# Kernel tuning notes

Measured on AMD Instinct MI355X. Metric: run time of the kernel, lower is better.

Reference implementation:

```python
import jax, jax.numpy as jnp
import numpy as np
from jax import lax

DN = ('NCHW', 'HWIO', 'NCHW')

def conv(x, w, b, stride, pad):
    y = lax.conv_general_dilated(x, w, (stride, stride), ((pad, pad), (pad, pad)),
                                 dimension_numbers=DN)
    return y + b[None, :, None, None]

def deconv(x, w, b):
    # PyTorch ConvTranspose2d(k=4, s=2, p=1) == conv with lhs_dilation=2, padding=k-1-p=2
    y = lax.conv_general_dilated(x, w, (1, 1), ((2, 2), (2, 2)), lhs_dilation=(2, 2),
                                 dimension_numbers=DN)
    return y + b[None, :, None, None]

def setup_inputs() -> dict:
    key = jax.random.key(0)
    ks = jax.random.split(key, 16)
    B, K, D = 4096, 512, 64
    def w(k, shape, fan_in):
        s = 1.0 / np.sqrt(fan_in)
        return jax.random.uniform(k, shape, jnp.float32, -s, s)
    return {
        'x': jax.random.uniform(ks[0], (B, 1, 28, 28), jnp.float32),
        # encoder
        'w1': w(ks[1], (4, 4, 1, 32), 4 * 4 * 1),  'b1': w(ks[2], (32,), 4 * 4 * 1),
        'w2': w(ks[3], (4, 4, 32, 64), 4 * 4 * 32), 'b2': w(ks[4], (64,), 4 * 4 * 32),
        'w3': w(ks[5], (1, 1, 64, D), 64),          'b3': w(ks[6], (D,), 64),
        # codebook, init uniform(-1/K, 1/K) as in the torch module
        'codebook': jax.random.uniform(ks[7], (K, D), jnp.float32, -1.0 / K, 1.0 / K),
        # decoder
        'dw0': w(ks[8], (1, 1, D, 64), D),          'db0': w(ks[9], (64,), D),
        'dw1': w(ks[10], (4, 4, 64, 32), 4 * 4 * 64), 'db1': w(ks[11], (32,), 4 * 4 * 64),
        'dw2': w(ks[12], (4, 4, 32, 1), 4 * 4 * 32),  'db2': w(ks[13], (1,), 4 * 4 * 32),
    }

def vector_quantize(z_perm, codebook, commitment_cost=0.25):
    # z_perm: [B, H, W, D]
    D = codebook.shape[1]
    flat_z = z_perm.reshape(-1, D)                                      # [N, D]
    dists = (jnp.sum(flat_z * flat_z, axis=1, keepdims=True)
             + jnp.sum(codebook * codebook, axis=1)
             - 2.0 * flat_z @ codebook.T)                               # [N, K]
    indices = jnp.argmin(dists, axis=1)                                 # [N]
    quantized = codebook[indices].reshape(z_perm.shape)                 # [B, H, W, D]
    e_latent = jnp.mean((quantized - lax.stop_gradient(z_perm)) ** 2)
    q_latent = jnp.mean((z_perm - lax.stop_gradient(quantized)) ** 2)
    vq_loss = e_latent + commitment_cost * q_latent
    quantized_st = z_perm + lax.stop_gradient(quantized - z_perm)
    return quantized_st, vq_loss, indices.reshape(z_perm.shape[:-1])

def reference(x, w1, b1, w2, b2, w3, b3, codebook, dw0, db0, dw1, db1, dw2, db2):
    # encoder: 28 -> 14 -> 7
    h = jax.nn.relu(conv(x, w1, b1, 2, 1))
    h = jax.nn.relu(conv(h, w2, b2, 2, 1))
    z = conv(h, w3, b3, 1, 0)                        # [B, D, 7, 7]
    z_perm = jnp.transpose(z, (0, 2, 3, 1))          # [B, 7, 7, D]
    zq_perm, vq_loss, indices = vector_quantize(z_perm, codebook)
    z_q = jnp.transpose(zq_perm, (0, 3, 1, 2))       # [B, D, 7, 7]
    # decoder: 7 -> 14 -> 28
    d = conv(z_q, dw0, db0, 1, 0)
    d = jax.nn.relu(deconv(d, dw1, db1))
    recon = jax.nn.sigmoid(deconv(d, dw2, db2))
    recon = recon[:, :, :28, :28]
    return recon, z, z_q, vq_loss, indices
```

## Files before the change

### kernel.cpp

```cpp
#include <hip/hip_runtime.h>


#define NB 4096

__device__ __forceinline__ float4 f4fma(float s, float4 w, float4 a) {
  a.x = fmaf(s, w.x, a.x); a.y = fmaf(s, w.y, a.y);
  a.z = fmaf(s, w.z, a.z); a.w = fmaf(s, w.w, a.w);
  return a;
}
__device__ __forceinline__ float4 f4relu(float4 a) {
  a.x = fmaxf(a.x, 0.f); a.y = fmaxf(a.y, 0.f);
  a.z = fmaxf(a.z, 0.f); a.w = fmaxf(a.w, 0.f);
  return a;
}
__device__ __forceinline__ float4 f4addrn(float4 a, float4 b) {
  a.x = __fadd_rn(a.x, b.x); a.y = __fadd_rn(a.y, b.y);
  a.z = __fadd_rn(a.z, b.z); a.w = __fadd_rn(a.w, b.w);
  return a;
}

__device__ __forceinline__ float np_sumsq64(const float* v) {
  float r[8];
#pragma unroll
  for (int j = 0; j < 8; ++j) r[j] = __fmul_rn(v[j], v[j]);
#pragma unroll
  for (int i = 8; i < 64; i += 8)
#pragma unroll
    for (int j = 0; j < 8; ++j) r[j] = __fadd_rn(r[j], __fmul_rn(v[i + j], v[i + j]));
  return __fadd_rn(__fadd_rn(__fadd_rn(r[0], r[1]), __fadd_rn(r[2], r[3])),
                   __fadd_rn(__fadd_rn(r[4], r[5]), __fadd_rn(r[6], r[7])));
}

__global__ __launch_bounds__(256) void k0_init(const float* __restrict__ cb,
                                               float* __restrict__ cn,
                                               float* __restrict__ loss) {
  int t = threadIdx.x;
  if (t == 0) *loss = 0.f;
  for (int k = t; k < 512; k += 256) cn[k] = np_sumsq64(&cb[k * 64]);
}

__global__ __launch_bounds__(256) void k1_conv1(const float* __restrict__ x,
                                                const float* __restrict__ w1,
                                                const float* __restrict__ b1,
                                                float* __restrict__ h1) {
  __shared__ float xs[784];
  __shared__ float wl[512];
  __shared__ float bs[32];
  int n = blockIdx.x, t = threadIdx.x;
  for (int j = t; j < 784; j += 256) xs[j] = x[n * 784 + j];
  for (int j = t; j < 512; j += 256) wl[j] = w1[j];
  if (t < 32) bs[t] = b1[t];
  __syncthreads();
  int c = t & 31, pg = t >> 5;
  for (int s = pg; s < 196; s += 8) {
    int oh = s / 14, ow = s % 14;
    float acc = 0.f;
#pragma unroll
    for (int kh = 0; kh < 4; ++kh) {
      int ih = 2 * oh - 1 + kh;
      if (ih < 0 || ih >= 28) continue;
#pragma unroll
      for (int kw = 0; kw < 4; ++kw) {
        int iw = 2 * ow - 1 + kw;
        if (iw < 0 || iw >= 28) continue;
        acc = fmaf(xs[ih * 28 + iw], wl[(kh * 4 + kw) * 32 + c], acc);
      }
    }
    acc = __fadd_rn(acc, bs[c]);
    h1[(n * 196 + s) * 32 + c] = fmaxf(acc, 0.f);
  }
}

__global__ __launch_bounds__(256) void k2_conv2(const float* __restrict__ h1,
                                                const float* __restrict__ w2,
                                                const float* __restrict__ b2,
                                                float* __restrict__ h2) {
  __shared__ float4 xs4[2 * 2049];
  int nb = blockIdx.x, t = threadIdx.x;
  size_t n0 = (size_t)nb * 2;
  for (int j = t; j < 4098; j += 256) xs4[j] = make_float4(0.f, 0.f, 0.f, 0.f);
  __syncthreads();
  for (int j = t; j < 1568; j += 256) {
    int p = j >> 3, c4 = j & 7;
    int ihp = p / 14 + 1, iwp = p % 14 + 1;
    int chunk = (c4 * 16 + ihp) * 16 + (iwp & 1) * 8 + (iwp >> 1);
    xs4[chunk] = *(const float4*)(h1 + n0 * 6272 + p * 32 + c4 * 4);
    xs4[2049 + chunk] = *(const float4*)(h1 + (n0 + 1) * 6272 + p * 32 + c4 * 4);
  }
  __syncthreads();
  int l = t & 63;
  int co0 = __builtin_amdgcn_readfirstlane((t >> 6) * 16);
  int img = l >> 5, pt = l & 31;
  int oh0 = pt >> 3, ow = pt & 7;
  int imgoff = img * 2049;
  bool v0 = (ow < 7);
  bool v1 = (ow < 7) && (oh0 + 4 < 7);
  float4 A0[4], A1[4];
#pragma unroll
  for (int g = 0; g < 4; ++g) { A0[g] = make_float4(0.f, 0.f, 0.f, 0.f); A1[g] = A0[g]; }
#pragma unroll 1
  for (int kk = 0; kk < 16; ++kk) {
    int kh = kk >> 2, kw = kk & 3;
    int cc = 2 * ow + kw; if (cc > 15) cc = 15;
    int off = (cc & 1) * 8 + (cc >> 1);
    int rc0 = 2 * oh0 + kh;
    int rc1 = rc0 + 8; if (rc1 > 15) rc1 = 15;
    int b0 = imgoff + rc0 * 16 + off;
    int b1 = imgoff + rc1 * 16 + off;
    int wb = __builtin_amdgcn_readfirstlane(kk * 2048 + co0);
#pragma unroll 2
    for (int c4 = 0; c4 < 8; ++c4) {
      float4 x0 = xs4[b0 + c4 * 256];
      float4 x1 = xs4[b1 + c4 * 256];
      float xa0[4] = {x0.x, x0.y, x0.z, x0.w};
      float xa1[4] = {x1.x, x1.y, x1.z, x1.w};
      const float* wk = w2 + wb + c4 * 256;
#pragma unroll
      for (int j = 0; j < 4; ++j) {
#pragma unroll
        for (int g = 0; g < 4; ++g) {
          float4 wv4;
          wv4.x = wk[j * 64 + g * 4 + 0]; wv4.y = wk[j * 64 + g * 4 + 1];
          wv4.z = wk[j * 64 + g * 4 + 2]; wv4.w = wk[j * 64 + g * 4 + 3];
          A0[g] = f4fma(xa0[j], wv4, A0[g]);
          A1[g] = f4fma(xa1[j], wv4, A1[g]);
        }
      }
    }
  }
  float4 bias[4];
#pragma unroll
  for (int g = 0; g < 4; ++g) bias[g] = *(const float4*)&b2[co0 + g * 4];
  if (v0) {
    size_t ob = ((n0 + img) * 49 + oh0 * 7 + ow) * 64 + co0;
#pragma unroll
    for (int g = 0; g < 4; ++g)
      *(float4*)&h2[ob + g * 4] = f4relu(f4addrn(A0[g], bias[g]));
  }
  if (v1) {
    size_t ob = ((n0 + img) * 49 + (oh0 + 4) * 7 + ow) * 64 + co0;
#pragma unroll
    for (int g = 0; g < 4; ++g)
      *(float4*)&h2[ob + g * 4] = f4relu(f4addrn(A1[g], bias[g]));
  }
}

__global__ __launch_bounds__(256) void k_pw(const float* __restrict__ xin,
                                            const float* __restrict__ w,
                                            const float* __restrict__ bias,
                                            float* __restrict__ yout) {
  __shared__ float tile[256 * 65];
  int t = threadIdx.x;
  long m0 = (long)blockIdx.x * 256;
  for (int j = t; j < 16384; j += 256) tile[(j >> 6) * 65 + (j & 63)] = xin[m0 * 64 + j];
  __syncthreads();
  float xr[64];
#pragma unroll
  for (int ci = 0; ci < 64; ++ci) xr[ci] = tile[t * 65 + ci];
  for (int g = 0; g < 4; ++g) {
    float4 z4 = make_float4(0.f, 0.f, 0.f, 0.f);
    float4 a0 = z4, a1 = z4, a2 = z4, a3 = z4;
#pragma unroll
    for (int ci = 0; ci < 64; ++ci) {
      float xv = xr[ci];
      const float* wr = &w[ci * 64 + g * 16];
      a0 = f4fma(xv, *(const float4*)&wr[0], a0);
      a1 = f4fma(xv, *(const float4*)&wr[4], a1);
      a2 = f4fma(xv, *(const float4*)&wr[8], a2);
      a3 = f4fma(xv, *(const float4*)&wr[12], a3);
    }
    a0 = f4addrn(a0, *(const float4*)&bias[g * 16 + 0]);
    a1 = f4addrn(a1, *(const float4*)&bias[g * 16 + 4]);
    a2 = f4addrn(a2, *(const float4*)&bias[g * 16 + 8]);
    a3 = f4addrn(a3, *(const float4*)&bias[g * 16 + 12]);
    float* dst = &tile[t * 65 + g * 16];
    dst[0] = a0.x; dst[1] = a0.y; dst[2] = a0.z; dst[3] = a0.w;
    dst[4] = a1.x; dst[5] = a1.y; dst[6] = a1.z; dst[7] = a1.w;
    dst[8] = a2.x; dst[9] = a2.y; dst[10] = a2.z; dst[11] = a2.w;
    dst[12] = a3.x; dst[13] = a3.y; dst[14] = a3.z; dst[15] = a3.w;
  }
  __syncthreads();
  for (int j = t; j < 16384; j += 256) yout[m0 * 64 + j] = tile[(j >> 6) * 65 + (j & 63)];
}

__global__ __launch_bounds__(128, 2) void k4_vq(const float* __restrict__ zin,
                                                const float* __restrict__ cb,
                                                const float* __restrict__ cn,
                                                float* __restrict__ zq_nhwc,
                                                float* __restrict__ outz,
                                                float* __restrict__ outzq,
                                                float* __restrict__ outidx,
                                                float* __restrict__ loss) {
  __shared__ float lds[8320];
  __shared__ float red[2];
  int t = threadIdx.x;
  size_t m0 = (size_t)blockIdx.x * 256;
  float zrA[64], zrB[64];

#define K4_STAGE_IN(S, ZR)                                                    \
  {                                                                           \
    __syncthreads();                                                          \
    const float* src = zin + (m0 + (S) * 128) * 64;                           \
    for (int j4 = t; j4 < 2048; j4 += 128) {                                  \
      int row = j4 >> 4, col = (j4 & 15) * 4;                                 \
      *(float4*)&lds[row * 65 + col] = *(const float4*)(src + j4 * 4);        \
    }                                                                         \
    __syncthreads();                                                          \
    _Pragma("unroll")                                                         \
    for (int ci = 0; ci < 64; ci += 4) {                                      \
      float4 v = *(float4*)&lds[t * 65 + ci];                                 \
      ZR[ci] = v.x; ZR[ci + 1] = v.y; ZR[ci + 2] = v.z; ZR[ci + 3] = v.w;     \
    }                                                                         \
  }

  K4_STAGE_IN(0, zrA)
  K4_STAGE_IN(1, zrB)

  float szA = np_sumsq64(zrA), szB = np_sumsq64(zrB);
  float minA = 3.4e38f, minB = 3.4e38f;
  int miA = 0, miB = 0;
#pragma unroll 1
  for (int ch = 0; ch < 8; ++ch) {
    __syncthreads();
    for (int j = t; j < 4096; j += 128) lds[j] = cb[ch * 4096 + j];
    if (ch == 0)
      for (int j = t; j < 512; j += 128) lds[4096 + j] = cn[j];
    __syncthreads();
#pragma unroll 1
    for (int k = 0; k < 64; k += 2) {
      const float* r0 = &lds[k * 64];
      const float* r1 = r0 + 64;
      float dA0 = 0.f, dA1 = 0.f, dB0 = 0.f, dB1 = 0.f;
#pragma unroll
      for (int ci = 0; ci < 64; ci += 4) {
        float4 c0 = *(const float4*)(r0 + ci);
        float4 c1 = *(const float4*)(r1 + ci);
        dA0 = fmaf(zrA[ci], c0.x, dA0); dA0 = fmaf(zrA[ci + 1], c0.y, dA0);
        dA0 = fmaf(zrA[ci + 2], c0.z, dA0); dA0 = fmaf(zrA[ci + 3], c0.w, dA0);
        dB0 = fmaf(zrB[ci], c0.x, dB0); dB0 = fmaf(zrB[ci + 1], c0.y, dB0);
        dB0 = fmaf(zrB[ci + 2], c0.z, dB0); dB0 = fmaf(zrB[ci + 3], c0.w, dB0);
        dA1 = fmaf(zrA[ci], c1.x, dA1); dA1 = fmaf(zrA[ci + 1], c1.y, dA1);
        dA1 = fmaf(zrA[ci + 2], c1.z, dA1); dA1 = fmaf(zrA[ci + 3], c1.w, dA1);
        dB1 = fmaf(zrB[ci], c1.x, dB1); dB1 = fmaf(zrB[ci + 1], c1.y, dB1);
        dB1 = fmaf(zrB[ci + 2], c1.z, dB1); dB1 = fmaf(zrB[ci + 3], c1.w, dB1);
      }
      float cn0 = lds[4096 + ch * 64 + k];
      float cn1 = lds[4096 + ch * 64 + k + 1];
      float qA0 = __fsub_rn(__fadd_rn(szA, cn0), __fmul_rn(2.f, dA0));
      float qA1 = __fsub_rn(__fadd_rn(szA, cn1), __fmul_rn(2.f, dA1));
      float qB0 = __fsub_rn(__fadd_rn(szB, cn0), __fmul_rn(2.f, dB0));
      float qB1 = __fsub_rn(__fadd_rn(szB, cn1), __fmul_rn(2.f, dB1));
      int kk = ch * 64 + k;
      if (qA0 < minA) { minA = qA0; miA = kk; }
      if (qA1 < minA) { minA = qA1; miA = kk + 1; }
      if (qB0 < minB) { minB = qB0; miB = kk; }
      if (qB1 < minB) { minB = qB1; miB = kk + 1; }
    }
  }

  outidx[m0 + t] = (float)miA;
  outidx[m0 + 128 + t] = (float)miB;
  {
    unsigned mA = (unsigned)(m0 + t), mB = (unsigned)(m0 + 128 + t);
    unsigned nA = mA / 49u, spA = mA % 49u;
    unsigned nB = mB / 49u, spB = mB % 49u;
    float* zoA = outz + (size_t)nA * 3136 + spA;
    float* zoB = outz + (size_t)nB * 3136 + spB;
#pragma unroll
    for (int ci = 0; ci < 64; ++ci) { zoA[ci * 49] = zrA[ci]; zoB[ci * 49] = zrB[ci]; }
  }

  float lsum = 0.f;
#define K4_STAGE_OUT(S, ZR, MI)                                               \
  {                                                                           \
    __syncthreads();                                                          \
    {                                                                         \
      unsigned mm = (unsigned)(m0 + (S) * 128 + t);                           \
      unsigned nn = mm / 49u, ss = mm % 49u;                                  \
      float* qo = outzq + (size_t)nn * 3136 + ss;                             \
      const float* qr = cb + (size_t)(MI) * 64;                               \
      _Pragma("unroll")                                                       \
      for (int ci = 0; ci < 64; ci += 4) {                                    \
        float4 q4 = *(const float4*)(qr + ci);                                \
        *(float4*)&lds[t * 65 + ci] = q4;                                     \
        qo[(ci + 0) * 49] = q4.x; qo[(ci + 1) * 49] = q4.y;                   \
        qo[(ci + 2) * 49] = q4.z; qo[(ci + 3) * 49] = q4.w;                   \
        float e0 = q4.x - ZR[ci], e1 = q4.y - ZR[ci + 1];                     \
        float e2 = q4.z - ZR[ci + 2], e3 = q4.w - ZR[ci + 3];                 \
        lsum = fmaf(e0, e0, lsum); lsum = fmaf(e1, e1, lsum);                 \
        lsum = fmaf(e2, e2, lsum); lsum = fmaf(e3, e3, lsum);                 \
      }                                                                       \
    }                                                                         \
    __syncthreads();                                                          \
    float* dstg = zq_nhwc + (m0 + (S) * 128) * 64;                            \
    for (int j4 = t; j4 < 2048; j4 += 128) {                                  \
      int row = j4 >> 4, col = (j4 & 15) * 4;                                 \
      *(float4*)(dstg + j4 * 4) = *(float4*)&lds[row * 65 + col];             \
    }                                                                         \
  }
  K4_STAGE_OUT(0, zrA, miA)
  K4_STAGE_OUT(1, zrB, miB)
#undef K4_STAGE_IN
#undef K4_STAGE_OUT
#pragma unroll
  for (int off = 32; off > 0; off >>= 1) lsum += __shfl_down(lsum, off);
  int wid = t >> 6, lane = t & 63;
  if (lane == 0) red[wid] = lsum;
  __syncthreads();
  if (t == 0) atomicAdd(loss, red[0] + red[1]);
}

__global__ __launch_bounds__(64) void k_lossfin(const float* __restrict__ loss,
                                                float* __restrict__ out) {
  if (threadIdx.x == 0) out[0] = loss[0] * (1.25f / 12845056.f);
}

__global__ __launch_bounds__(256) void k6_deconv1(const float* __restrict__ d0,
                                                  const float* __restrict__ dw1,
                                                  const float* __restrict__ db1,
                                                  float* __restrict__ d1) {
  __shared__ float4 xs4[2 * 1297];
  int nb = blockIdx.x, t = threadIdx.x;
  size_t n0 = (size_t)nb * 2;
  for (int j = t; j < 2594; j += 256) xs4[j] = make_float4(0.f, 0.f, 0.f, 0.f);
  __syncthreads();
  for (int j = t; j < 784; j += 256) {
    int p = j >> 4, c4 = j & 15;
    int chunk = c4 * 81 + (p / 7 + 1) * 9 + (p % 7 + 1);
    xs4[chunk] = *(const float4*)(d0 + n0 * 3136 + p * 64 + c4 * 4);
    xs4[1297 + chunk] = *(const float4*)(d0 + (n0 + 1) * 3136 + p * 64 + c4 * 4);
  }
  __syncthreads();
  int l = t & 63;
  int ph = __builtin_amdgcn_readfirstlane(t >> 6);
  int ra = ph >> 1, rb = ph & 1;
  int img = l >> 5, pt = l & 31;
  bool v1 = (pt + 32 < 49);
  int p1 = v1 ? pt + 32 : 48;
  int mh0 = pt / 7, mw0 = pt % 7;
  int mh1 = p1 / 7, mw1 = p1 % 7;
  int imgoff = img * 1297;
  float4 A0[8], A1[8];
#pragma unroll
  for (int g = 0; g < 8; ++g) { A0[g] = make_float4(0.f, 0.f, 0.f, 0.f); A1[g] = A0[g]; }
#pragma unroll 1
  for (int tap = 0; tap < 4; ++tap) {
    int th = tap >> 1, tw = tap & 1;
    int kh = 2 * th + ra, kw = 2 * tw + rb;
    int b0 = imgoff + (mh0 + th + ra) * 9 + (mw0 + tw + rb);
    int b1 = imgoff + (mh1 + th + ra) * 9 + (mw1 + tw + rb);
    int wb = __builtin_amdgcn_readfirstlane((kh * 4 + kw) * 2048);
#pragma unroll 1
    for (int c4 = 0; c4 < 16; ++c4) {
      float4 x0 = xs4[b0 + c4 * 81];
      float4 x1 = xs4[b1 + c4 * 81];
      float xa0[4] = {x0.x, x0.y, x0.z, x0.w};
      float xa1[4] = {x1.x, x1.y, x1.z, x1.w};
      const float* wk = dw1 + wb + c4 * 128;
#pragma unroll
      for (int j = 0; j < 4; ++j) {
#pragma unroll
        for (int g = 0; g < 8; ++g) {
          float4 wv4;
          wv4.x = wk[j * 32 + g * 4 + 0]; wv4.y = wk[j * 32 + g * 4 + 1];
          wv4.z = wk[j * 32 + g * 4 + 2]; wv4.w = wk[j * 32 + g * 4 + 3];
          A0[g] = f4fma(xa0[j], wv4, A0[g]);
          A1[g] = f4fma(xa1[j], wv4, A1[g]);
        }
      }
    }
  }
  int oh0 = 2 * mh0 + ra, ow0 = 2 * mw0 + rb;
  size_t ob0 = ((n0 + img) * 196 + (size_t)(oh0 * 14 + ow0)) * 32;
#pragma unroll
  for (int g = 0; g < 8; ++g) {
    float4 bg = *(const float4*)&db1[g * 4];
    *(float4*)&d1[ob0 + g * 4] = f4relu(f4addrn(A0[g], bg));
  }
  if (v1) {
    int oh1 = 2 * mh1 + ra, ow1 = 2 * mw1 + rb;
    size_t ob1 = ((n0 + img) * 196 + (size_t)(oh1 * 14 + ow1)) * 32;
#pragma unroll
    for (int g = 0; g < 8; ++g) {
      float4 bg = *(const float4*)&db1[g * 4];
      *(float4*)&d1[ob1 + g * 4] = f4relu(f4addrn(A1[g], bg));
    }
  }
}

__global__ __launch_bounds__(256) void k7_deconv2(const float* __restrict__ d1,
                                                  const float* __restrict__ dw2,
                                                  const float* __restrict__ db2,
                                                  float* __restrict__ recon) {
  __shared__ float xs[196 * 36];
  __shared__ float wl[512];
  int n = blockIdx.x, t = threadIdx.x;
  for (int j = t; j < 6272; j += 256) xs[(j >> 5) * 36 + (j & 31)] = d1[(size_t)n * 6272 + j];
  for (int j = t; j < 512; j += 256) wl[j] = dw2[j];
  __syncthreads();
  float bias = db2[0];
  for (int j = t; j < 392; j += 256) {
    int ra = j / 196, rem = j % 196;
    int mh = rem / 14, mw = rem % 14;
    float acc0 = bias, acc1 = bias;
    bool vm = (mw >= 1), vp = (mw + 1 < 14);
#pragma unroll
    for (int th = 0; th < 2; ++th) {
      int ih = mh + th - 1 + ra;
      if (ih < 0 || ih >= 14) continue;
      int kh = 2 * th + ra;
#pragma unroll
      for (int ci = 0; ci < 32; ci += 4) {
        float4 z4 = make_float4(0.f, 0.f, 0.f, 0.f);
        float4 xm = vm ? *(float4*)&xs[(ih * 14 + mw - 1) * 36 + ci] : z4;
        float4 x0 = *(float4*)&xs[(ih * 14 + mw) * 36 + ci];
        float4 xp = vp ? *(float4*)&xs[(ih * 14 + mw + 1) * 36 + ci] : z4;
        float4 wk0 = *(float4*)&wl[(kh * 4 + 0) * 32 + ci];
        float4 wk1 = *(float4*)&wl[(kh * 4 + 1) * 32 + ci];
        float4 wk2 = *(float4*)&wl[(kh * 4 + 2) * 32 + ci];
        float4 wk3 = *(float4*)&wl[(kh * 4 + 3) * 32 + ci];
        acc0 = fmaf(xm.x, wk0.x, acc0); acc0 = fmaf(xm.y, wk0.y, acc0);
        acc0 = fmaf(xm.z, wk0.z, acc0); acc0 = fmaf(xm.w, wk0.w, acc0);
        acc0 = fmaf(x0.x, wk2.x, acc0); acc0 = fmaf(x0.y, wk2.y, acc0);
        acc0 = fmaf(x0.z, wk2.z, acc0); acc0 = fmaf(x0.w, wk2.w, acc0);
        acc1 = fmaf(x0.x, wk1.x, acc1); acc1 = fmaf(x0.y, wk1.y, acc1);
        acc1 = fmaf(x0.z, wk1.z, acc1); acc1 = fmaf(x0.w, wk1.w, acc1);
        acc1 = fmaf(xp.x, wk3.x, acc1); acc1 = fmaf(xp.y, wk3.y, acc1);
        acc1 = fmaf(xp.z, wk3.z, acc1); acc1 = fmaf(xp.w, wk3.w, acc1);
      }
    }
    float r0 = 1.f / (1.f + __expf(-acc0));
    float r1 = 1.f / (1.f + __expf(-acc1));
    int oh = 2 * mh + ra;
    *(float2*)&recon[(size_t)n * 784 + oh * 28 + 2 * mw] = make_float2(r0, r1);
  }
}

extern "C" void kernel_launch(void* const* d_in, const int* in_sizes, int n_in,
                              void* d_out, int out_size, void* d_ws, size_t ws_size,
                              hipStream_t stream) {
  const float* x   = (const float*)d_in[0];
  const float* w1  = (const float*)d_in[1];
  const float* b1  = (const float*)d_in[2];
  const float* w2  = (const float*)d_in[3];
  const float* b2  = (const float*)d_in[4];
  const float* w3  = (const float*)d_in[5];
  const float* b3  = (const float*)d_in[6];
  const float* cb  = (const float*)d_in[7];
  const float* dw0 = (const float*)d_in[8];
  const float* db0 = (const float*)d_in[9];
  const float* dw1 = (const float*)d_in[10];
  const float* db1 = (const float*)d_in[11];
  const float* dw2 = (const float*)d_in[12];
  const float* db2 = (const float*)d_in[13];
  float* out = (float*)d_out;
  float* ws  = (float*)d_ws;

  float* h1   = ws;
  float* h2   = ws + 25690112;
  float* zb   = ws + 38535168;
  float* cn   = ws + 51380224;
  float* loss = ws + 51380736;

  float* recon   = out;
  float* zout    = out + 3211264;
  float* zqout   = out + 16056320;
  float* lossout = out + 28901376;
  float* idxout  = out + 28901377;

  k0_init<<<1, 256, 0, stream>>>(cb, cn, loss);
  k1_conv1<<<NB, 256, 0, stream>>>(x, w1, b1, h1);
  k2_conv2<<<NB / 2, 256, 0, stream>>>(h1, w2, b2, h2);
  k_pw<<<784, 256, 0, stream>>>(h2, w3, b3, zb);
  k4_vq<<<784, 128, 0, stream>>>(zb, cb, cn, h2, zout, zqout, idxout, loss);
  k_lossfin<<<1, 64, 0, stream>>>(loss, lossout);
  k_pw<<<784, 256, 0, stream>>>(h2, dw0, db0, zb);
  k6_deconv1<<<NB / 2, 256, 0, stream>>>(zb, dw1, db1, h1);
  k7_deconv2<<<NB, 256, 0, stream>>>(h1, dw2, db2, recon);
}
```

Baseline: 1.102 ms.

## Split codebook reads between LDS and direct global loads in VQ kernel

The VQ argmin loop now stages only the even codebook rows of each chunk into LDS, using float4 copies, and reads the odd rows straight from global memory (cache) through a uniform pointer. Codebook norms are loaded into LDS once before the loop instead of inside chunk 0. The aim is to halve LDS footprint and staging traffic per chunk, which could raise occupancy and split load bandwidth between LDS and the scalar/vector cache. The risk is added global load latency inside the inner loop. The LDS region used to stage z rows is also reused for the norms after an added barrier.

```diff
diff --git a/kernel.cpp b/kernel.cpp
--- a/kernel.cpp
+++ b/kernel.cpp
@@ -216,20 +216,25 @@
   K4_STAGE_IN(0, zrA)
   K4_STAGE_IN(1, zrB)
 
+  __syncthreads();
+  *(float4*)&lds[2048 + t * 4] = *(const float4*)&cn[t * 4];
+
   float szA = np_sumsq64(zrA), szB = np_sumsq64(zrB);
   float minA = 3.4e38f, minB = 3.4e38f;
   int miA = 0, miB = 0;
 #pragma unroll 1
   for (int ch = 0; ch < 8; ++ch) {
     __syncthreads();
-    for (int j = t; j < 4096; j += 128) lds[j] = cb[ch * 4096 + j];
-    if (ch == 0)
-      for (int j = t; j < 512; j += 128) lds[4096 + j] = cn[j];
+    for (int j4 = t; j4 < 512; j4 += 128) {
+      int e = j4 >> 4, c4 = (j4 & 15) * 4;
+      *(float4*)&lds[e * 64 + c4] =
+          *(const float4*)&cb[(ch * 64 + 2 * e) * 64 + c4];
+    }
     __syncthreads();
 #pragma unroll 1
-    for (int k = 0; k < 64; k += 2) {
-      const float* r0 = &lds[k * 64];
-      const float* r1 = r0 + 64;
+    for (int kk = 0; kk < 32; ++kk) {
+      const float* r0 = &lds[kk * 64];
+      const float* r1 = cb + (ch * 64 + 2 * kk + 1) * 64;
       float dA0 = 0.f, dA1 = 0.f, dB0 = 0.f, dB1 = 0.f;
 #pragma unroll
       for (int ci = 0; ci < 64; ci += 4) {
@@ -244,17 +249,17 @@
         dB1 = fmaf(zrB[ci], c1.x, dB1); dB1 = fmaf(zrB[ci + 1], c1.y, dB1);
         dB1 = fmaf(zrB[ci + 2], c1.z, dB1); dB1 = fmaf(zrB[ci + 3], c1.w, dB1);
       }
-      float cn0 = lds[4096 + ch * 64 + k];
-      float cn1 = lds[4096 + ch * 64 + k + 1];
+      int kkg = ch * 64 + 2 * kk;
+      float cn0 = lds[2048 + kkg];
+      float cn1 = lds[2048 + kkg + 1];
       float qA0 = __fsub_rn(__fadd_rn(szA, cn0), __fmul_rn(2.f, dA0));
       float qA1 = __fsub_rn(__fadd_rn(szA, cn1), __fmul_rn(2.f, dA1));
       float qB0 = __fsub_rn(__fadd_rn(szB, cn0), __fmul_rn(2.f, dB0));
       float qB1 = __fsub_rn(__fadd_rn(szB, cn1), __fmul_rn(2.f, dB1));
-      int kk = ch * 64 + k;
-      if (qA0 < minA) { minA = qA0; miA = kk; }
-      if (qA1 < minA) { minA = qA1; miA = kk + 1; }
-      if (qB0 < minB) { minB = qB0; miB = kk; }
-      if (qB1 < minB) { minB = qB1; miB = kk + 1; }
+      if (qA0 < minA) { minA = qA0; miA = kkg; }
+      if (qA1 < minA) { minA = qA1; miA = kkg + 1; }
+      if (qB0 < minB) { minB = qB0; miB = kkg; }
+      if (qB1 < minB) { minB = qB1; miB = kkg + 1; }
     }
   }
 
```

Result: slower. 1.212 ms (+10.0%).
